# Kernel optimization log

Measured on AMD Instinct MI355X. Metric: run time of the kernel, lower is better.

Reference implementation:

```python
import jax, jax.numpy as jnp
import numpy as np
import math

D_MODEL = 768
H = 12
D_K = D_MODEL // H
KSIZE = 3  # 2*suppression_radius+1


def setup_inputs() -> dict:
    key = jax.random.key(0)
    ks = jax.random.split(key, 12)
    B, S = 8, 1024
    s = 1.0 / math.sqrt(D_MODEL)
    return {
        "q": jax.random.normal(ks[0], (B, S, D_MODEL), jnp.float32),
        "k": jax.random.normal(ks[1], (B, S, D_MODEL), jnp.float32),
        "v": jax.random.normal(ks[2], (B, S, D_MODEL), jnp.float32),
        "wq": jax.random.normal(ks[3], (D_MODEL, D_MODEL), jnp.float32) * s,
        "bq": jnp.zeros((D_MODEL,), jnp.float32),
        "wk": jax.random.normal(ks[4], (D_MODEL, D_MODEL), jnp.float32) * s,
        "bk": jnp.zeros((D_MODEL,), jnp.float32),
        "wv": jax.random.normal(ks[5], (D_MODEL, D_MODEL), jnp.float32) * s,
        "bv": jnp.zeros((D_MODEL,), jnp.float32),
        "wo": jax.random.normal(ks[6], (D_MODEL, D_MODEL), jnp.float32) * s,
        "bo": jnp.zeros((D_MODEL,), jnp.float32),
        "conv_w": jax.random.normal(ks[7], (H, 1, KSIZE, KSIZE), jnp.float32) * 0.1,
    }


def reference(q, k, v, wq, bq, wk, bk, wv, bv, wo, bo, conv_w):
    B, S, _ = q.shape
    # projections -> [B, h, S, d_k]
    Q = (q @ wq.T + bq).reshape(B, S, H, D_K).transpose(0, 2, 1, 3)
    K = (k @ wk.T + bk).reshape(B, S, H, D_K).transpose(0, 2, 1, 3)
    V = (v @ wv.T + bv).reshape(B, S, H, D_K).transpose(0, 2, 1, 3)
    scale = 1.0 / math.sqrt(D_K)
    scores = jnp.einsum("bhqd,bhkd->bhqk", Q, K) * scale  # [B,h,S,S]
    # per-head depthwise 3x3 conv over the score "image" (SAME padding, no bias)
    supp = jax.lax.conv_general_dilated(
        scores, conv_w, window_strides=(1, 1), padding="SAME",
        dimension_numbers=("NCHW", "OIHW", "NCHW"), feature_group_count=H)
    probs = jax.nn.softmax(scores - supp, axis=-1)
    out = jnp.einsum("bhqk,bhkd->bhqd", probs, V)
    out = out.transpose(0, 2, 1, 3).reshape(B, S, D_MODEL)
    return out @ wo.T + bo
```

## Files before the change

kernel.cpp:

```cpp
#include <hip/hip_runtime.h>
#include <math.h>

typedef __attribute__((ext_vector_type(8))) short short8;
typedef __attribute__((ext_vector_type(4))) float f32x4;
typedef __attribute__((ext_vector_type(4))) unsigned short ushort4v;

#define D_MODEL 768
#define NH      12
#define DK      64
#define SEQ     1024
#define NB      8
#define MTOT    (NB*SEQ)
#define NELT    ((size_t)MTOT*D_MODEL)
#define WELT    ((size_t)D_MODEL*D_MODEL)

__device__ __forceinline__ unsigned short f2bf(float f) {
    unsigned int u = __builtin_bit_cast(unsigned int, f);
    unsigned int r = (u + 0x7FFFu + ((u >> 16) & 1u)) >> 16;
    return (unsigned short)r;
}
__device__ __forceinline__ float bf2f(unsigned short h) {
    return __builtin_bit_cast(float, ((unsigned int)h) << 16);
}
__device__ __forceinline__ void gload_lds16(const void* g, void* lds) {
    __builtin_amdgcn_global_load_lds(
        (const __attribute__((address_space(1))) unsigned int*)g,
        (__attribute__((address_space(3))) unsigned int*)lds, 16, 0, 0);
}

__global__ __launch_bounds__(256) void cvt3(
    const float* __restrict__ a, const float* __restrict__ b, const float* __restrict__ c,
    unsigned short* __restrict__ oa, unsigned short* __restrict__ ob, unsigned short* __restrict__ oc)
{
    size_t i = (size_t)blockIdx.x * 256 + threadIdx.x;
    const size_t per = NELT / 8;
    const float* s; unsigned short* d; size_t l;
    if (i < per)            { s = a; d = oa; l = i; }
    else if (i < 2*per)     { s = b; d = ob; l = i - per; }
    else                    { s = c; d = oc; l = i - 2*per; }
    const float4* sp = (const float4*)(s + l*8);
    float4 v0 = sp[0], v1 = sp[1];
    short8 o;
    o[0]=(short)f2bf(v0.x); o[1]=(short)f2bf(v0.y); o[2]=(short)f2bf(v0.z); o[3]=(short)f2bf(v0.w);
    o[4]=(short)f2bf(v1.x); o[5]=(short)f2bf(v1.y); o[6]=(short)f2bf(v1.z); o[7]=(short)f2bf(v1.w);
    *(short8*)(d + l*8) = o;
}

__global__ __launch_bounds__(256) void cvt4(
    const float* __restrict__ a, const float* __restrict__ b,
    const float* __restrict__ c, const float* __restrict__ e,
    unsigned short* __restrict__ oa, unsigned short* __restrict__ ob,
    unsigned short* __restrict__ oc, unsigned short* __restrict__ oe)
{
    size_t i = (size_t)blockIdx.x * 256 + threadIdx.x;
    const size_t per = WELT / 8;
    const float* s; unsigned short* d; size_t l;
    if (i < per)        { s = a; d = oa; l = i; }
    else if (i < 2*per) { s = b; d = ob; l = i - per; }
    else if (i < 3*per) { s = c; d = oc; l = i - 2*per; }
    else                { s = e; d = oe; l = i - 3*per; }
    const float4* sp = (const float4*)(s + l*8);
    float4 v0 = sp[0], v1 = sp[1];
    short8 o;
    o[0]=(short)f2bf(v0.x); o[1]=(short)f2bf(v0.y); o[2]=(short)f2bf(v0.z); o[3]=(short)f2bf(v0.w);
    o[4]=(short)f2bf(v1.x); o[5]=(short)f2bf(v1.y); o[6]=(short)f2bf(v1.z); o[7]=(short)f2bf(v1.w);
    *(short8*)(d + l*8) = o;
}

#define BM 128
#define BN 128
#define BKG 64

template<int MODE>
__global__ __launch_bounds__(256) void gemm_bf16(
    const unsigned short* __restrict__ A, const unsigned short* __restrict__ W,
    const float* __restrict__ bias, void* __restrict__ Cout, float scale)
{
    __shared__ unsigned short As[BM*BKG];
    __shared__ unsigned short Bs[BN*BKG];
    const int tid = threadIdx.x;
    const int lane = tid & 63, wid = tid >> 6;
    const int wr = wid >> 1, wc = wid & 1;
    const int m0 = blockIdx.y * BM, n0 = blockIdx.x * BN;

    f32x4 acc[4][4];
    #pragma unroll
    for (int i = 0; i < 4; ++i)
        #pragma unroll
        for (int j = 0; j < 4; ++j) acc[i][j] = (f32x4)(0.f);

    for (int k0 = 0; k0 < D_MODEL; k0 += BKG) {
        __syncthreads();
        #pragma unroll
        for (int j = 0; j < 4; ++j) {
            int p = ((wid*4 + j) << 9) + lane*8;
            int row = p >> 6, off = p & 63;
            const unsigned short* srcA = A + (size_t)(m0+row)*D_MODEL + k0 + (off ^ ((row&7)<<3));
            gload_lds16(srcA, &As[(wid*4 + j) << 9]);
            const unsigned short* srcB = W + (size_t)(n0+row)*D_MODEL + k0 + (off ^ ((row&7)<<3));
            gload_lds16(srcB, &Bs[(wid*4 + j) << 9]);
        }
        __syncthreads();
        #pragma unroll
        for (int ks = 0; ks < 2; ++ks) {
            short8 af[4], bf8[4];
            #pragma unroll
            for (int mi = 0; mi < 4; ++mi) {
                int row = wr*64 + mi*16 + (lane & 15);
                af[mi] = *(const short8*)&As[row*BKG + ((ks*32 + (lane>>4)*8) ^ ((row&7)<<3))];
            }
            #pragma unroll
            for (int ni = 0; ni < 4; ++ni) {
                int row = wc*64 + ni*16 + (lane & 15);
                bf8[ni] = *(const short8*)&Bs[row*BKG + ((ks*32 + (lane>>4)*8) ^ ((row&7)<<3))];
            }
            #pragma unroll
            for (int mi = 0; mi < 4; ++mi)
                #pragma unroll
                for (int ni = 0; ni < 4; ++ni)
                    acc[mi][ni] = __builtin_amdgcn_mfma_f32_16x16x32_bf16(af[mi], bf8[ni], acc[mi][ni], 0, 0, 0);
        }
    }

    float bv[4];
    #pragma unroll
    for (int ni = 0; ni < 4; ++ni) bv[ni] = bias[n0 + wc*64 + ni*16 + (lane & 15)];

    if (MODE == 0) {
        unsigned short* C = (unsigned short*)Cout;
        #pragma unroll
        for (int mi = 0; mi < 4; ++mi)
            #pragma unroll
            for (int ni = 0; ni < 4; ++ni) {
                int col = n0 + wc*64 + ni*16 + (lane & 15);
                int rbase = m0 + wr*64 + mi*16 + ((lane>>4)<<2);
                #pragma unroll
                for (int j = 0; j < 4; ++j)
                    C[(size_t)(rbase+j)*D_MODEL + col] = f2bf((acc[mi][ni][j] + bv[ni]) * scale);
            }
    } else if (MODE == 1) {
        unsigned short* C = (unsigned short*)Cout;
        #pragma unroll
        for (int mi = 0; mi < 4; ++mi)
            #pragma unroll
            for (int ni = 0; ni < 4; ++ni) {
                int col = n0 + wc*64 + ni*16 + (lane & 15);
                int hh = col >> 6, dd = col & 63;
                int m = m0 + wr*64 + mi*16 + ((lane>>4)<<2);
                int bb = m >> 10, ss = m & (SEQ-1);
                ushort4v pk;
                #pragma unroll
                for (int j = 0; j < 4; ++j) pk[j] = f2bf(acc[mi][ni][j] + bv[ni]);
                *(ushort4v*)&C[((size_t)(bb*NH + hh)*DK + dd)*SEQ + ss] = pk;
            }
    } else {
        float* C = (float*)Cout;
        #pragma unroll
        for (int mi = 0; mi < 4; ++mi)
            #pragma unroll
            for (int ni = 0; ni < 4; ++ni) {
                int col = n0 + wc*64 + ni*16 + (lane & 15);
                int rbase = m0 + wr*64 + mi*16 + ((lane>>4)<<2);
                #pragma unroll
                for (int j = 0; j < 4; ++j)
                    C[(size_t)(rbase+j)*D_MODEL + col] = acc[mi][ni][j] + bv[ni];
            }
    }
}

#define KVB 64
#define NCH (SEQ/KVB)

__global__ __launch_bounds__(512, 4) void attn_flash(
    const unsigned short* __restrict__ Qp,
    const unsigned short* __restrict__ Kp,
    const unsigned short* __restrict__ Vt,
    const float* __restrict__ CW,
    unsigned short* __restrict__ Aop)
{
    __shared__ unsigned short Ks[2][66*64];
    __shared__ unsigned short Vs[2][64*64];
    __shared__ unsigned short UB[130*64];

    const int tid = threadIdx.x;
    const int lane = tid & 63, wid = tid >> 6;
    const int lq = lane & 15, lg = lane >> 4;

    const int bid = blockIdx.x;
    const int sw = (bid & 7) * 96 + (bid >> 3);
    const int q0 = (sw & 7) * 128;
    const int bh = sw >> 3;
    const int h = bh % NH, b = bh / NH;

    float wcv[9];
    #pragma unroll
    for (int i = 0; i < 9; ++i) wcv[i] = CW[h*9 + i];

    const unsigned short* KpB = Kp + (size_t)b*SEQ*D_MODEL + h*DK;
    const unsigned short* QpB = Qp + (size_t)b*SEQ*D_MODEL + h*DK;
    const char* VtB = (const char*)Vt + (size_t)bh*DK*SEQ*2;

    short8 kr0, kr1;
    auto kload = [&](int ck) {
        { int r = tid >> 3, oct = tid & 7;
          int gk = ck*KVB - 1 + r;
          short8 v = (short8)0;
          if (gk >= 0 && gk < SEQ) v = *(const short8*)&KpB[(size_t)gk*D_MODEL + oct*8];
          kr0 = v; }
        if (tid < 16) {
          int r = 64 + (tid >> 3), oct = tid & 7;
          int gk = ck*KVB - 1 + r;
          short8 v = (short8)0;
          if (gk >= 0 && gk < SEQ) v = *(const short8*)&KpB[(size_t)gk*D_MODEL + oct*8];
          kr1 = v; }
    };
    auto kstore = [&](int buf) {
        { int r = tid >> 3, oct = tid & 7;
          *(short8*)&Ks[buf][r*64 + ((oct ^ (r&7)) << 3)] = kr0; }
        if (tid < 16) {
          int r = 64 + (tid >> 3), oct = tid & 7;
          *(short8*)&Ks[buf][r*64 + ((oct ^ (r&7)) << 3)] = kr1; }
    };
    auto vstage = [&](int ck, int buf) {
        int p = tid * 16;
        int row = p >> 7, off = p & 127;
        const char* src = VtB + ((size_t)row*SEQ + ck*KVB)*2 + (off ^ ((row&7)<<4));
        gload_lds16(src, (char*)Vs[buf] + p);
    };

    kload(0);

    {
        short8 qs0 = (short8)0, qs1 = (short8)0, qs2 = (short8)0;
        int r0 = tid >> 3, o0 = tid & 7;
        int g0 = q0 - 1 + r0;
        if (g0 >= 0 && g0 < SEQ) qs0 = *(const short8*)&QpB[(size_t)g0*D_MODEL + o0*8];
        int r1 = (512 + tid) >> 3, o1 = tid & 7;
        int g1 = q0 - 1 + r1;
        if (g1 >= 0 && g1 < SEQ) qs1 = *(const short8*)&QpB[(size_t)g1*D_MODEL + o1*8];
        int r2 = 0, o2 = 0, g2 = -1;
        if (tid < 16) {
            r2 = (1024 + tid) >> 3; o2 = tid & 7;
            g2 = q0 - 1 + r2;
            if (g2 >= 0 && g2 < SEQ) qs2 = *(const short8*)&QpB[(size_t)g2*D_MODEL + o2*8];
        }
        *(short8*)&UB[r0*64 + ((o0 ^ (r0&7)) << 3)] = qs0;
        *(short8*)&UB[r1*64 + ((o1 ^ (r1&7)) << 3)] = qs1;
        if (tid < 16) *(short8*)&UB[r2*64 + ((o2 ^ (r2&7)) << 3)] = qs2;
    }
    __syncthreads();

    short8 qtf0[2], qtf1[2], qtf2[2];
    {
        int r0 = wid*16 + lq;
        #pragma unroll
        for (int ks = 0; ks < 2; ++ks) {
            int oct = ks*4 + lg;
            int ra = r0, rb = r0 + 1, rc = r0 + 2;
            short8 am = *(const short8*)&UB[ra*64 + ((oct ^ (ra&7)) << 3)];
            short8 ac = *(const short8*)&UB[rb*64 + ((oct ^ (rb&7)) << 3)];
            short8 ap = *(const short8*)&UB[rc*64 + ((oct ^ (rc&7)) << 3)];
            short8 f0, f1, f2;
            #pragma unroll
            for (int j = 0; j < 8; ++j) {
                float fm = bf2f((unsigned short)am[j]);
                float fc = bf2f((unsigned short)ac[j]);
                float fp = bf2f((unsigned short)ap[j]);
                float t0 = fc - (wcv[1]*fm + wcv[4]*fc + wcv[7]*fp);
                float t1 = -(wcv[0]*fm + wcv[3]*fc + wcv[6]*fp);
                float t2 = -(wcv[2]*fm + wcv[5]*fc + wcv[8]*fp);
                f0[j] = (short)f2bf(t0);
                f1[j] = (short)f2bf(t1);
                f2[j] = (short)f2bf(t2);
            }
            qtf0[ks] = f0; qtf1[ks] = f1; qtf2[ks] = f2;
        }
    }
    kstore(0);
    vstage(0, 0);
    __syncthreads();

    unsigned short* Pw = &UB[wid * 1024];

    float m = -1e30f, l = 0.f;
    f32x4 oac[4];
    #pragma unroll
    for (int dt = 0; dt < 4; ++dt) oac[dt] = (f32x4)(0.f);

    int cur = 0;
    for (int ck = 0; ck < NCH; ++ck) {
        if (ck < NCH-1) { kload(ck+1); vstage(ck+1, cur^1); }

        f32x4 st[4];
        #pragma unroll
        for (int t = 0; t < 4; ++t) {
            f32x4 s = (f32x4)(0.f);
            #pragma unroll
            for (int ks = 0; ks < 2; ++ks) {
                int oct = ks*4 + lg;
                int ar0 = t*16 + lq + 1;
                short8 a0 = *(const short8*)&Ks[cur][ar0*64 + ((oct ^ (ar0&7)) << 3)];
                s = __builtin_amdgcn_mfma_f32_16x16x32_bf16(a0, qtf0[ks], s, 0, 0, 0);
                int ar1 = t*16 + lq;
                short8 a1 = *(const short8*)&Ks[cur][ar1*64 + ((oct ^ (ar1&7)) << 3)];
                s = __builtin_amdgcn_mfma_f32_16x16x32_bf16(a1, qtf1[ks], s, 0, 0, 0);
                int ar2 = t*16 + lq + 2;
                short8 a2 = *(const short8*)&Ks[cur][ar2*64 + ((oct ^ (ar2&7)) << 3)];
                s = __builtin_amdgcn_mfma_f32_16x16x32_bf16(a2, qtf2[ks], s, 0, 0, 0);
            }
            st[t] = s;
        }

        float tmax = -1e30f;
        #pragma unroll
        for (int t = 0; t < 4; ++t)
            #pragma unroll
            for (int j = 0; j < 4; ++j) tmax = fmaxf(tmax, st[t][j]);
        tmax = fmaxf(tmax, __shfl_xor(tmax, 16));
        tmax = fmaxf(tmax, __shfl_xor(tmax, 32));
        float mn = fmaxf(m, tmax);
        float r = __expf(m - mn);
        float lsum = 0.f;
        #pragma unroll
        for (int t = 0; t < 4; ++t)
            #pragma unroll
            for (int j = 0; j < 4; ++j) {
                float e = __expf(st[t][j] - mn);
                st[t][j] = e;
                lsum += e;
            }
        lsum += __shfl_xor(lsum, 16);
        lsum += __shfl_xor(lsum, 32);
        l = l * r + lsum;
        m = mn;
        #pragma unroll
        for (int dt = 0; dt < 4; ++dt)
            #pragma unroll
            for (int j = 0; j < 4; ++j) oac[dt][j] *= r;

        #pragma unroll
        for (int t = 0; t < 4; ++t) {
            ushort4v pk;
            #pragma unroll
            for (int j = 0; j < 4; ++j) pk[j] = f2bf(st[t][j]);
            *(ushort4v*)&Pw[lq*64 + ((t*16 + lg*4) ^ ((lq&7)<<3))] = pk;
        }
        #pragma unroll
        for (int kk = 0; kk < 2; ++kk) {
            short8 p8 = *(const short8*)&Pw[lq*64 + ((kk*32 + lg*8) ^ ((lq&7)<<3))];
            #pragma unroll
            for (int dt = 0; dt < 4; ++dt) {
                int vr = dt*16 + lq;
                int voct = kk*4 + lg;
                short8 v8 = *(const short8*)&Vs[cur][vr*64 + ((voct ^ (vr&7)) << 3)];
                oac[dt] = __builtin_amdgcn_mfma_f32_16x16x32_bf16(v8, p8, oac[dt], 0, 0, 0);
            }
        }

        if (ck < NCH-1) kstore(cur^1);
        __syncthreads();
        cur ^= 1;
    }

    float invl = 1.0f / l;
    int qg = q0 + wid*16 + lq;
    #pragma unroll
    for (int dt = 0; dt < 4; ++dt) {
        ushort4v o;
        #pragma unroll
        for (int j = 0; j < 4; ++j) o[j] = f2bf(oac[dt][j] * invl);
        *(ushort4v*)&Aop[(size_t)(b*SEQ + qg)*D_MODEL + h*DK + dt*16 + lg*4] = o;
    }
}

extern "C" void kernel_launch(void* const* d_in, const int* in_sizes, int n_in,
                              void* d_out, int out_size, void* d_ws, size_t ws_size,
                              hipStream_t stream)
{
    const float* q  = (const float*)d_in[0];
    const float* k  = (const float*)d_in[1];
    const float* v  = (const float*)d_in[2];
    const float* wq = (const float*)d_in[3];
    const float* bq = (const float*)d_in[4];
    const float* wk = (const float*)d_in[5];
    const float* bk = (const float*)d_in[6];
    const float* wv = (const float*)d_in[7];
    const float* bv = (const float*)d_in[8];
    const float* wo = (const float*)d_in[9];
    const float* bo = (const float*)d_in[10];
    const float* cw = (const float*)d_in[11];

    unsigned short* qb  = (unsigned short*)d_ws;
    unsigned short* kb  = qb  + NELT;
    unsigned short* vb  = kb  + NELT;
    unsigned short* wqb = vb  + NELT;
    unsigned short* wkb = wqb + WELT;
    unsigned short* wvb = wkb + WELT;
    unsigned short* wob = wvb + WELT;
    unsigned short* Qp  = wob + WELT;
    unsigned short* Kp  = Qp  + NELT;
    unsigned short* Vtp = Kp  + NELT;
    unsigned short* Aop = Vtp + NELT;

    cvt3<<<(int)(3*NELT/8/256), 256, 0, stream>>>(q, k, v, qb, kb, vb);
    cvt4<<<(int)(4*WELT/8/256), 256, 0, stream>>>(wq, wk, wv, wo, wqb, wkb, wvb, wob);

    dim3 gg(D_MODEL/BN, MTOT/BM);
    gemm_bf16<0><<<gg, 256, 0, stream>>>(qb, wqb, bq, Qp, 0.125f);
    gemm_bf16<0><<<gg, 256, 0, stream>>>(kb, wkb, bk, Kp, 1.0f);
    gemm_bf16<1><<<gg, 256, 0, stream>>>(vb, wvb, bv, Vtp, 1.0f);

    attn_flash<<<dim3(768), 512, 0, stream>>>(Qp, Kp, Vtp, cw, Aop);

    gemm_bf16<2><<<gg, 256, 0, stream>>>(Aop, wob, bo, (float*)d_out, 1.0f);
}
```

Measured before the change: 172.6 us.

## Fuse input fp32→bf16 conversion into projection GEMM, batch QKV, lazy softmax rescale

Removes the standalone cvt3 pass: the projection GEMM now loads fp32 activations into registers, converts them to bf16 and writes them into swizzled LDS, prefetching the next K tile. The three Q/K/V projections are merged into one launch using blockIdx.z. The attention softmax switches to exp2 by folding log2(e) into the conv-adjusted K operand, and it skips rescaling the accumulators unless the running max grows by more than a threshold. This saves a full read and write of the bf16 activation copies and some launch and exp overhead, at the cost of register-staged A loads in the GEMM and larger un-rescaled exponent ranges.

```diff
diff --git a/kernel.cpp b/kernel.cpp
--- a/kernel.cpp
+++ b/kernel.cpp
@@ -13,6 +13,7 @@
 #define MTOT    (NB*SEQ)
 #define NELT    ((size_t)MTOT*D_MODEL)
 #define WELT    ((size_t)D_MODEL*D_MODEL)
+#define L2E     1.44269504088896f
 
 __device__ __forceinline__ unsigned short f2bf(float f) {
     unsigned int u = __builtin_bit_cast(unsigned int, f);
@@ -26,24 +27,6 @@
     __builtin_amdgcn_global_load_lds(
         (const __attribute__((address_space(1))) unsigned int*)g,
         (__attribute__((address_space(3))) unsigned int*)lds, 16, 0, 0);
-}
-
-__global__ __launch_bounds__(256) void cvt3(
-    const float* __restrict__ a, const float* __restrict__ b, const float* __restrict__ c,
-    unsigned short* __restrict__ oa, unsigned short* __restrict__ ob, unsigned short* __restrict__ oc)
-{
-    size_t i = (size_t)blockIdx.x * 256 + threadIdx.x;
-    const size_t per = NELT / 8;
-    const float* s; unsigned short* d; size_t l;
-    if (i < per)            { s = a; d = oa; l = i; }
-    else if (i < 2*per)     { s = b; d = ob; l = i - per; }
-    else                    { s = c; d = oc; l = i - 2*per; }
-    const float4* sp = (const float4*)(s + l*8);
-    float4 v0 = sp[0], v1 = sp[1];
-    short8 o;
-    o[0]=(short)f2bf(v0.x); o[1]=(short)f2bf(v0.y); o[2]=(short)f2bf(v0.z); o[3]=(short)f2bf(v0.w);
-    o[4]=(short)f2bf(v1.x); o[5]=(short)f2bf(v1.y); o[6]=(short)f2bf(v1.z); o[7]=(short)f2bf(v1.w);
-    *(short8*)(d + l*8) = o;
 }
 
 __global__ __launch_bounds__(256) void cvt4(
@@ -71,10 +54,13 @@
 #define BN 128
 #define BKG 64
 
-template<int MODE>
-__global__ __launch_bounds__(256) void gemm_bf16(
-    const unsigned short* __restrict__ A, const unsigned short* __restrict__ W,
-    const float* __restrict__ bias, void* __restrict__ Cout, float scale)
+__global__ __launch_bounds__(256) void proj_gemm(
+    const float* __restrict__ Aq, const float* __restrict__ Ak, const float* __restrict__ Av,
+    const unsigned short* __restrict__ Wq, const unsigned short* __restrict__ Wk,
+    const unsigned short* __restrict__ Wv,
+    const float* __restrict__ bq, const float* __restrict__ bk, const float* __restrict__ bv,
+    unsigned short* __restrict__ Qp, unsigned short* __restrict__ Kp,
+    unsigned short* __restrict__ Vtp)
 {
     __shared__ unsigned short As[BM*BKG];
     __shared__ unsigned short Bs[BN*BKG];
@@ -82,6 +68,115 @@
     const int lane = tid & 63, wid = tid >> 6;
     const int wr = wid >> 1, wc = wid & 1;
     const int m0 = blockIdx.y * BM, n0 = blockIdx.x * BN;
+    const int z = blockIdx.z;
+
+    const float* A          = (z == 0) ? Aq : (z == 1) ? Ak : Av;
+    const unsigned short* W = (z == 0) ? Wq : (z == 1) ? Wk : Wv;
+    const float* bias       = (z == 0) ? bq : (z == 1) ? bk : bv;
+
+    f32x4 acc[4][4];
+    #pragma unroll
+    for (int i = 0; i < 4; ++i)
+        #pragma unroll
+        for (int j = 0; j < 4; ++j) acc[i][j] = (f32x4)(0.f);
+
+    const int arow = tid >> 1, ahalf = (tid & 1) * 32;
+    float areg[32];
+    auto aload = [&](int k0) {
+        const float* src = A + (size_t)(m0 + arow)*D_MODEL + k0 + ahalf;
+        #pragma unroll
+        for (int i = 0; i < 8; ++i)
+            *(float4*)&areg[i*4] = *(const float4*)(src + i*4);
+    };
+    auto astore = [&]() {
+        #pragma unroll
+        for (int j = 0; j < 4; ++j) {
+            int oct = (ahalf >> 3) + j;
+            short8 v;
+            #pragma unroll
+            for (int e = 0; e < 8; ++e) v[e] = (short)f2bf(areg[j*8 + e]);
+            *(short8*)&As[arow*64 + ((oct ^ (arow&7)) << 3)] = v;
+        }
+    };
+
+    aload(0);
+    for (int k0 = 0; k0 < D_MODEL; k0 += BKG) {
+        __syncthreads();
+        astore();
+        #pragma unroll
+        for (int j = 0; j < 4; ++j) {
+            int p = ((wid*4 + j) << 9) + lane*8;
+            int row = p >> 6, off = p & 63;
+            const unsigned short* srcB = W + (size_t)(n0+row)*D_MODEL + k0 + (off ^ ((row&7)<<3));
+            gload_lds16(srcB, &Bs[(wid*4 + j) << 9]);
+        }
+        __syncthreads();
+        if (k0 + BKG < D_MODEL) aload(k0 + BKG);
+        #pragma unroll
+        for (int ks = 0; ks < 2; ++ks) {
+            short8 af[4], bf8[4];
+            #pragma unroll
+            for (int mi = 0; mi < 4; ++mi) {
+                int row = wr*64 + mi*16 + (lane & 15);
+                af[mi] = *(const short8*)&As[row*BKG + ((ks*32 + (lane>>4)*8) ^ ((row&7)<<3))];
+            }
+            #pragma unroll
+            for (int ni = 0; ni < 4; ++ni) {
+                int row = wc*64 + ni*16 + (lane & 15);
+                bf8[ni] = *(const short8*)&Bs[row*BKG + ((ks*32 + (lane>>4)*8) ^ ((row&7)<<3))];
+            }
+            #pragma unroll
+            for (int mi = 0; mi < 4; ++mi)
+                #pragma unroll
+                for (int ni = 0; ni < 4; ++ni)
+                    acc[mi][ni] = __builtin_amdgcn_mfma_f32_16x16x32_bf16(af[mi], bf8[ni], acc[mi][ni], 0, 0, 0);
+        }
+    }
+
+    float bv4[4];
+    #pragma unroll
+    for (int ni = 0; ni < 4; ++ni) bv4[ni] = bias[n0 + wc*64 + ni*16 + (lane & 15)];
+
+    if (z < 2) {
+        unsigned short* C = (z == 0) ? Qp : Kp;
+        const float scale = (z == 0) ? 0.125f : 1.0f;
+        #pragma unroll
+        for (int mi = 0; mi < 4; ++mi)
+            #pragma unroll
+            for (int ni = 0; ni < 4; ++ni) {
+                int col = n0 + wc*64 + ni*16 + (lane & 15);
+                int rbase = m0 + wr*64 + mi*16 + ((lane>>4)<<2);
+                #pragma unroll
+                for (int j = 0; j < 4; ++j)
+                    C[(size_t)(rbase+j)*D_MODEL + col] = f2bf((acc[mi][ni][j] + bv4[ni]) * scale);
+            }
+    } else {
+        #pragma unroll
+        for (int mi = 0; mi < 4; ++mi)
+            #pragma unroll
+            for (int ni = 0; ni < 4; ++ni) {
+                int col = n0 + wc*64 + ni*16 + (lane & 15);
+                int hh = col >> 6, dd = col & 63;
+                int m = m0 + wr*64 + mi*16 + ((lane>>4)<<2);
+                int bb = m >> 10, ss = m & (SEQ-1);
+                ushort4v pk;
+                #pragma unroll
+                for (int j = 0; j < 4; ++j) pk[j] = f2bf(acc[mi][ni][j] + bv4[ni]);
+                *(ushort4v*)&Vtp[((size_t)(bb*NH + hh)*DK + dd)*SEQ + ss] = pk;
+            }
+    }
+}
+
+__global__ __launch_bounds__(256) void gemm_out(
+    const unsigned short* __restrict__ A, const unsigned short* __restrict__ W,
+    const float* __restrict__ bias, float* __restrict__ C)
+{
+    __shared__ unsigned short As[BM*BKG];
+    __shared__ unsigned short Bs[BN*BKG];
+    const int tid = threadIdx.x;
+    const int lane = tid & 63, wid = tid >> 6;
+    const int wr = wid >> 1, wc = wid & 1;
+    const int m0 = blockIdx.y * BM, n0 = blockIdx.x * BN;
 
     f32x4 acc[4][4];
     #pragma unroll
@@ -122,54 +217,25 @@
         }
     }
 
-    float bv[4];
-    #pragma unroll
-    for (int ni = 0; ni < 4; ++ni) bv[ni] = bias[n0 + wc*64 + ni*16 + (lane & 15)];
-
-    if (MODE == 0) {
-        unsigned short* C = (unsigned short*)Cout;
-        #pragma unroll
-        for (int mi = 0; mi < 4; ++mi)
-            #pragma unroll
-            for (int ni = 0; ni < 4; ++ni) {
-                int col = n0 + wc*64 + ni*16 + (lane & 15);
-                int rbase = m0 + wr*64 + mi*16 + ((lane>>4)<<2);
-                #pragma unroll
-                for (int j = 0; j < 4; ++j)
-                    C[(size_t)(rbase+j)*D_MODEL + col] = f2bf((acc[mi][ni][j] + bv[ni]) * scale);
-            }
-    } else if (MODE == 1) {
-        unsigned short* C = (unsigned short*)Cout;
-        #pragma unroll
-        for (int mi = 0; mi < 4; ++mi)
-            #pragma unroll
-            for (int ni = 0; ni < 4; ++ni) {
-                int col = n0 + wc*64 + ni*16 + (lane & 15);
-                int hh = col >> 6, dd = col & 63;
-                int m = m0 + wr*64 + mi*16 + ((lane>>4)<<2);
-                int bb = m >> 10, ss = m & (SEQ-1);
-                ushort4v pk;
-                #pragma unroll
-                for (int j = 0; j < 4; ++j) pk[j] = f2bf(acc[mi][ni][j] + bv[ni]);
-                *(ushort4v*)&C[((size_t)(bb*NH + hh)*DK + dd)*SEQ + ss] = pk;
-            }
-    } else {
-        float* C = (float*)Cout;
-        #pragma unroll
-        for (int mi = 0; mi < 4; ++mi)
-            #pragma unroll
-            for (int ni = 0; ni < 4; ++ni) {
-                int col = n0 + wc*64 + ni*16 + (lane & 15);
-                int rbase = m0 + wr*64 + mi*16 + ((lane>>4)<<2);
-                #pragma unroll
-                for (int j = 0; j < 4; ++j)
-                    C[(size_t)(rbase+j)*D_MODEL + col] = acc[mi][ni][j] + bv[ni];
-            }
-    }
+    float bv4[4];
+    #pragma unroll
+    for (int ni = 0; ni < 4; ++ni) bv4[ni] = bias[n0 + wc*64 + ni*16 + (lane & 15)];
+
+    #pragma unroll
+    for (int mi = 0; mi < 4; ++mi)
+        #pragma unroll
+        for (int ni = 0; ni < 4; ++ni) {
+            int col = n0 + wc*64 + ni*16 + (lane & 15);
+            int rbase = m0 + wr*64 + mi*16 + ((lane>>4)<<2);
+            #pragma unroll
+            for (int j = 0; j < 4; ++j)
+                C[(size_t)(rbase+j)*D_MODEL + col] = acc[mi][ni][j] + bv4[ni];
+        }
 }
 
 #define KVB 64
 #define NCH (SEQ/KVB)
+#define THR 8.0f
 
 __global__ __launch_bounds__(512, 4) void attn_flash(
     const unsigned short* __restrict__ Qp,
@@ -266,9 +332,9 @@
                 float fm = bf2f((unsigned short)am[j]);
                 float fc = bf2f((unsigned short)ac[j]);
                 float fp = bf2f((unsigned short)ap[j]);
-                float t0 = fc - (wcv[1]*fm + wcv[4]*fc + wcv[7]*fp);
-                float t1 = -(wcv[0]*fm + wcv[3]*fc + wcv[6]*fp);
-                float t2 = -(wcv[2]*fm + wcv[5]*fc + wcv[8]*fp);
+                float t0 = (fc - (wcv[1]*fm + wcv[4]*fc + wcv[7]*fp)) * L2E;
+                float t1 = -(wcv[0]*fm + wcv[3]*fc + wcv[6]*fp) * L2E;
+                float t2 = -(wcv[2]*fm + wcv[5]*fc + wcv[8]*fp) * L2E;
                 f0[j] = (short)f2bf(t0);
                 f1[j] = (short)f2bf(t1);
                 f2[j] = (short)f2bf(t2);
@@ -318,25 +384,29 @@
             for (int j = 0; j < 4; ++j) tmax = fmaxf(tmax, st[t][j]);
         tmax = fmaxf(tmax, __shfl_xor(tmax, 16));
         tmax = fmaxf(tmax, __shfl_xor(tmax, 32));
-        float mn = fmaxf(m, tmax);
-        float r = __expf(m - mn);
+
+        if (!__all(tmax - m <= THR)) {
+            float mn = fmaxf(m, tmax);
+            float r = exp2f(m - mn);
+            l *= r;
+            #pragma unroll
+            for (int dt = 0; dt < 4; ++dt)
+                #pragma unroll
+                for (int j = 0; j < 4; ++j) oac[dt][j] *= r;
+            m = mn;
+        }
         float lsum = 0.f;
         #pragma unroll
         for (int t = 0; t < 4; ++t)
             #pragma unroll
             for (int j = 0; j < 4; ++j) {
-                float e = __expf(st[t][j] - mn);
+                float e = exp2f(st[t][j] - m);
                 st[t][j] = e;
                 lsum += e;
             }
         lsum += __shfl_xor(lsum, 16);
         lsum += __shfl_xor(lsum, 32);
-        l = l * r + lsum;
-        m = mn;
-        #pragma unroll
-        for (int dt = 0; dt < 4; ++dt)
-            #pragma unroll
-            for (int j = 0; j < 4; ++j) oac[dt][j] *= r;
+        l += lsum;
 
         #pragma unroll
         for (int t = 0; t < 4; ++t) {
@@ -390,10 +460,7 @@
     const float* bo = (const float*)d_in[10];
     const float* cw = (const float*)d_in[11];
 
-    unsigned short* qb  = (unsigned short*)d_ws;
-    unsigned short* kb  = qb  + NELT;
-    unsigned short* vb  = kb  + NELT;
-    unsigned short* wqb = vb  + NELT;
+    unsigned short* wqb = (unsigned short*)d_ws;
     unsigned short* wkb = wqb + WELT;
     unsigned short* wvb = wkb + WELT;
     unsigned short* wob = wvb + WELT;
@@ -402,15 +469,12 @@
     unsigned short* Vtp = Kp  + NELT;
     unsigned short* Aop = Vtp + NELT;
 
-    cvt3<<<(int)(3*NELT/8/256), 256, 0, stream>>>(q, k, v, qb, kb, vb);
     cvt4<<<(int)(4*WELT/8/256), 256, 0, stream>>>(wq, wk, wv, wo, wqb, wkb, wvb, wob);
 
-    dim3 gg(D_MODEL/BN, MTOT/BM);
-    gemm_bf16<0><<<gg, 256, 0, stream>>>(qb, wqb, bq, Qp, 0.125f);
-    gemm_bf16<0><<<gg, 256, 0, stream>>>(kb, wkb, bk, Kp, 1.0f);
-    gemm_bf16<1><<<gg, 256, 0, stream>>>(vb, wvb, bv, Vtp, 1.0f);
+    dim3 gg(D_MODEL/BN, MTOT/BM, 3);
+    proj_gemm<<<gg, 256, 0, stream>>>(q, k, v, wqb, wkb, wvb, bq, bk, bv, Qp, Kp, Vtp);
 
     attn_flash<<<dim3(768), 512, 0, stream>>>(Qp, Kp, Vtp, cw, Aop);
 
-    gemm_bf16<2><<<gg, 256, 0, stream>>>(Aop, wob, bo, (float*)d_out, 1.0f);
-}
+    gemm_out<<<dim3(D_MODEL/BN, MTOT/BM), 256, 0, stream>>>(Aop, wob, bo, (float*)d_out);
+}
```

Result: slower. 200.9 us (+16.4%).
